# Kernel optimization log

Measured on AMD Instinct MI355X. Metric: run time of the kernel, lower is better.

## Reference

```python
import jax, jax.numpy as jnp
import numpy as np

B = 8192
EPS = 1e-5


def _bn(x, g, b):
    # BatchNorm1d in training mode: biased batch statistics
    m = jnp.mean(x, axis=0)
    v = jnp.mean((x - m) ** 2, axis=0)
    return g * (x - m) * jax.lax.rsqrt(v + EPS) + b


def setup_inputs() -> dict:
    key = jax.random.key(0)
    ks = jax.random.split(key, 24)
    w = lambda k, shape: jax.random.normal(k, shape, jnp.float32) * 0.02
    z = lambda shape: jnp.zeros(shape, jnp.float32)
    o = lambda shape: jnp.ones(shape, jnp.float32)
    inp = {"pred_vertices": jax.random.normal(ks[0], (B, 1723, 3), jnp.float32)}
    inp["W0"] = w(ks[1], (5169, 1024)); inp["b0"] = z(1024); inp["g0"] = o(1024); inp["be0"] = z(1024)
    inp["W1a"] = w(ks[2], (1024, 1024)); inp["b1a"] = z(1024); inp["g1a"] = o(1024); inp["be1a"] = z(1024)
    inp["W1b"] = w(ks[3], (1024, 1024)); inp["b1b"] = z(1024); inp["g1b"] = o(1024); inp["be1b"] = z(1024)
    inp["W2a"] = w(ks[4], (1024, 1024)); inp["b2a"] = z(1024); inp["g2a"] = o(1024); inp["be2a"] = z(1024)
    inp["W2b"] = w(ks[5], (1024, 1024)); inp["b2b"] = z(1024); inp["g2b"] = o(1024); inp["be2b"] = z(1024)
    inp["W3"] = w(ks[6], (1024, 226)); inp["b3"] = z(226)
    return inp


def reference(pred_vertices, W0, b0, g0, be0,
              W1a, b1a, g1a, be1a, W1b, b1b, g1b, be1b,
              W2a, b2a, g2a, be2a, W2b, b2b, g2b, be2b,
              W3, b3):
    bsz = pred_vertices.shape[0]
    x = pred_vertices.reshape(bsz, 1723 * 3)
    # FCBlock: Linear -> BN -> ReLU
    h = jax.nn.relu(_bn(x @ W0 + b0, g0, be0))
    # FCResBlock x2: relu(x + BN(Linear(relu(BN(Linear(x))))))
    t = jax.nn.relu(_bn(h @ W1a + b1a, g1a, be1a))
    t = _bn(t @ W1b + b1b, g1b, be1b)
    h = jax.nn.relu(h + t)
    t = jax.nn.relu(_bn(h @ W2a + b2a, g2a, be2a))
    t = _bn(t @ W2b + b2b, g2b, be2b)
    h = jax.nn.relu(h + t)
    out = h @ W3 + b3  # (B, 226)
    rot = out[:, :216].reshape(-1, 3, 3)  # (B*24, 3, 3)
    pred_betas = out[:, 216:]
    # Batched Procrustes orthogonalization: R = U V^T, then scale by det (no-grad)
    U, S, Vh = jnp.linalg.svd(rot, full_matrices=False)
    R = jnp.einsum('nij,njk->nik', U, Vh)
    det = jax.lax.stop_gradient(jnp.linalg.det(R))[:, None, None]
    pred_rotmat = (R * det).reshape(bsz, 24, 3, 3)
    return (pred_rotmat, pred_betas)
```

## Files before the change

kernel.cpp:

```cpp
#include <hip/hip_runtime.h>
#include <hip/hip_bf16.h>
#include <math.h>

typedef __attribute__((ext_vector_type(8))) _Float16 half8;
typedef __attribute__((ext_vector_type(4))) float floatx4;
typedef __attribute__((ext_vector_type(4))) unsigned short ushortx4;

__device__ __forceinline__ float hu2f(unsigned short u) {
    _Float16 h;
    __builtin_memcpy(&h, &u, 2);
    return (float)h;
}
__device__ __forceinline__ unsigned short f2hu(float x) {
    _Float16 h = (_Float16)x;
    unsigned short u;
    __builtin_memcpy(&u, &h, 2);
    return u;
}
__device__ __forceinline__ void split2(float a, unsigned short& s0,
                                       unsigned short& s1) {
    s0 = f2hu(a);
    float r1 = a - hu2f(s0);
    s1 = f2hu(r1);
}

typedef __attribute__((address_space(1))) unsigned int as1_u32;
typedef __attribute__((address_space(3))) unsigned int as3_u32;
__device__ __forceinline__ void gload16(const void* g, void* l) {
    __builtin_amdgcn_global_load_lds((const as1_u32*)g, (as3_u32*)l, 16, 0, 0);
}

__global__ __launch_bounds__(256) void wsplit2_kernel(
    const float* __restrict__ W, unsigned short* __restrict__ out,
    int Ktrue, int Kpad, int Ntrue, int Nalloc)
{
    __shared__ float T[32][33];
    const int tx = threadIdx.x & 31, ty = threadIdx.x >> 5;
    const int k0 = blockIdx.x * 32, n0 = blockIdx.y * 32;
#pragma unroll
    for (int i = 0; i < 4; i++) {
        int k = k0 + ty + 8 * i, n = n0 + tx;
        T[ty + 8 * i][tx] = (k < Ktrue && n < Ntrue) ? W[(size_t)k * Ntrue + n] : 0.f;
    }
    __syncthreads();
    const size_t PS = (size_t)Nalloc * Kpad;
#pragma unroll
    for (int i = 0; i < 4; i++) {
        int n = n0 + ty + 8 * i, k = k0 + tx;
        if (n < Nalloc) {
            unsigned short h0, h1;
            split2(T[tx][ty + 8 * i], h0, h1);
            size_t base = (size_t)n * Kpad + k;
            out[base] = h0;
            out[PS + base] = h1;
        }
    }
}

__global__ __launch_bounds__(256) void asplit2_kernel(
    const float* __restrict__ A, unsigned short* __restrict__ out,
    int Ka, int Kpad, int M)
{
    const int kq = Kpad >> 2;
    const int n = M * kq;
    int idx = blockIdx.x * 256 + threadIdx.x;
    if (idx >= n) return;
    int row = idx / kq, c4 = idx - row * kq;
    const size_t PS = (size_t)M * Kpad;
    ushortx4 o0, o1;
#pragma unroll
    for (int e = 0; e < 4; e++) {
        int col = c4 * 4 + e;
        float v = (col < Ka) ? A[(size_t)row * Ka + col] : 0.f;
        unsigned short a, b;
        split2(v, a, b);
        o0[e] = a; o1[e] = b;
    }
    size_t base = (size_t)row * Kpad + c4 * 4;
    *(ushortx4*)(out + base) = o0;
    *(ushortx4*)(out + PS + base) = o1;
}

__global__ __launch_bounds__(256, 3) void mfma_gemm_h(
    const unsigned short* __restrict__ Apl,
    const unsigned short* __restrict__ Bpl,
    const float* __restrict__ bias, float* __restrict__ C,
    float* __restrict__ part,
    int M, int N, int Kpad, int Nb)
{
    __shared__ __align__(16) unsigned short As[2][128][32];
    __shared__ __align__(16) unsigned short Bs[2][128][32];
    __shared__ float sstat[2][4][16][2];

    const int tid = threadIdx.x;
    const int lane = tid & 63;
    const int wave = tid >> 6;
    const int wm = (wave & 1) * 64, wn = (wave >> 1) * 64;

    const int gx = gridDim.x;
    const int nwg = gx * gridDim.y;
    const int id = blockIdx.y * gx + blockIdx.x;
    const int cpx = nwg >> 3;
    const int swz = (id & 7) * cpx + (id >> 3);
    const int bm = (swz / gx) * 128, bn = (swz % gx) * 128;

    const int l15 = lane & 15, q = lane >> 4;
    const size_t PSA = (size_t)M * Kpad;
    const size_t PSB = (size_t)Nb * Kpad;

    const int srow = lane >> 2;
    const int gslot = (lane & 3) ^ ((srow >> 1) & 3);
    const int rkey = (l15 >> 1) & 3;

    floatx4 acc[4][4] = {};

    for (int k0 = 0; k0 < Kpad; k0 += 32) {
#pragma unroll
        for (int i = 0; i < 8; i++) {
            int e = wave * 8 + i;
            int mat = e >> 4, p = (e >> 3) & 1, rb = (e & 7) << 4;
            if (mat == 0) {
                gload16(Apl + (size_t)p * PSA + (size_t)(bm + rb + srow) * Kpad
                            + (k0 + gslot * 8),
                        &As[p][rb][0]);
            } else {
                gload16(Bpl + (size_t)p * PSB + (size_t)(bn + rb + srow) * Kpad
                            + (k0 + gslot * 8),
                        &Bs[p][rb][0]);
            }
        }
        __syncthreads();

        half8 bfr[2][4];
#pragma unroll
        for (int p = 0; p < 2; p++)
#pragma unroll
            for (int ni = 0; ni < 4; ni++)
                bfr[p][ni] = *(const half8*)&Bs[p][wn + ni * 16 + l15][(q ^ rkey) * 8];
#pragma unroll
        for (int pa = 0; pa < 2; pa++) {
            half8 af[4];
#pragma unroll
            for (int mi = 0; mi < 4; mi++)
                af[mi] = *(const half8*)&As[pa][wm + mi * 16 + l15][(q ^ rkey) * 8];
#pragma unroll
            for (int pb = 0; pb + pa < 2; pb++) {
#pragma unroll
                for (int mi = 0; mi < 4; mi++)
#pragma unroll
                    for (int ni = 0; ni < 4; ni++)
                        acc[mi][ni] = __builtin_amdgcn_mfma_f32_16x16x32_f16(
                            af[mi], bfr[pb][ni], acc[mi][ni], 0, 0, 0);
            }
        }
        __syncthreads();
    }

    float ps[4], ps2[4];
#pragma unroll
    for (int ni = 0; ni < 4; ni++) {
        int col = bn + wn + ni * 16 + l15;
        float s = 0.f, s2 = 0.f;
        if (col < N) {
            float bv = bias[col];
#pragma unroll
            for (int mi = 0; mi < 4; mi++) {
#pragma unroll
                for (int reg = 0; reg < 4; reg++) {
                    int row = bm + wm + mi * 16 + q * 4 + reg;
                    float v = acc[mi][ni][reg] + bv;
                    C[(size_t)row * N + col] = v;
                    s += v;
                    s2 += v * v;
                }
            }
        }
        ps[ni] = s; ps2[ni] = s2;
    }

    if (part) {
#pragma unroll
        for (int ni = 0; ni < 4; ni++) {
            ps[ni]  += __shfl_xor(ps[ni], 16);  ps[ni]  += __shfl_xor(ps[ni], 32);
            ps2[ni] += __shfl_xor(ps2[ni], 16); ps2[ni] += __shfl_xor(ps2[ni], 32);
        }
        if (q == 0 && (wave & 1) == 1) {
#pragma unroll
            for (int ni = 0; ni < 4; ni++) {
                sstat[wave >> 1][ni][l15][0] = ps[ni];
                sstat[wave >> 1][ni][l15][1] = ps2[ni];
            }
        }
        __syncthreads();
        if (q == 0 && (wave & 1) == 0) {
            int chunk = bm >> 7;
#pragma unroll
            for (int ni = 0; ni < 4; ni++) {
                int col = bn + wn + ni * 16 + l15;
                float s  = ps[ni]  + sstat[wave >> 1][ni][l15][0];
                float s2 = ps2[ni] + sstat[wave >> 1][ni][l15][1];
                part[(size_t)(chunk * 2 + 0) * N + col] = s;
                part[(size_t)(chunk * 2 + 1) * N + col] = s2;
            }
        }
    }
}

template <bool AVEC, bool NV4>
__global__ __launch_bounds__(256) void gemm128(
    const float* __restrict__ A, const float* __restrict__ B,
    const float* __restrict__ bias, float* __restrict__ C,
    int M, int N, int Keff, int Ktrue, int Ka)
{
    __shared__ __align__(16) float Asm[16][132];
    __shared__ __align__(16) float Bsm[16][132];
    const int tid = threadIdx.x;
    const int bm = blockIdx.y * 128, bn = blockIdx.x * 128;
    const int tx = tid & 15, ty = tid >> 4;
    const int arow = tid >> 2, ac = tid & 3;
    const int bk = tid >> 4, bc = tid & 15;
    float acc[8][8] = {};
    for (int k0 = 0; k0 < Keff; k0 += 16) {
#pragma unroll
        for (int h = 0; h < 2; h++) {
            int rr = arow + h * 64;
            if (AVEC) {
                float4 v = *(const float4*)&A[(size_t)(bm + rr) * Ka + k0 + ac * 4];
                const float* pv = &v.x;
#pragma unroll
                for (int e = 0; e < 4; e++) Asm[ac * 4 + e][rr] = pv[e];
            } else {
#pragma unroll
                for (int e = 0; e < 4; e++) {
                    int kg = k0 + ac * 4 + e;
                    Asm[ac * 4 + e][rr] = (kg < Ka) ? A[(size_t)(bm + rr) * Ka + kg] : 0.f;
                }
            }
        }
        {
            int kg = k0 + bk;
            bool kok = (kg < Ktrue);
#pragma unroll
            for (int h = 0; h < 2; h++) {
                int cc = bc * 4 + h * 64;
                if (NV4) {
                    float4 v = {0.f, 0.f, 0.f, 0.f};
                    if (kok) v = *(const float4*)&B[(size_t)kg * N + bn + cc];
                    *(float4*)&Bsm[bk][cc] = v;
                } else {
#pragma unroll
                    for (int e = 0; e < 4; e++) {
                        int col = bn + cc + e;
                        Bsm[bk][cc + e] = (kok && col < N) ? B[(size_t)kg * N + col] : 0.f;
                    }
                }
            }
        }
        __syncthreads();
#pragma unroll
        for (int k = 0; k < 16; k++) {
            float4 a0 = *(const float4*)&Asm[k][ty * 4];
            float4 a1 = *(const float4*)&Asm[k][ty * 4 + 64];
            float4 b0 = *(const float4*)&Bsm[k][tx * 4];
            float4 b1 = *(const float4*)&Bsm[k][tx * 4 + 64];
            float av[8] = {a0.x, a0.y, a0.z, a0.w, a1.x, a1.y, a1.z, a1.w};
            float bv[8] = {b0.x, b0.y, b0.z, b0.w, b1.x, b1.y, b1.z, b1.w};
#pragma unroll
            for (int i = 0; i < 8; i++)
#pragma unroll
                for (int j = 0; j < 8; j++) acc[i][j] += av[i] * bv[j];
        }
        __syncthreads();
    }
#pragma unroll
    for (int i = 0; i < 8; i++) {
        int row = bm + (i < 4 ? ty * 4 + i : 64 + ty * 4 + (i - 4));
#pragma unroll
        for (int jh = 0; jh < 2; jh++)
#pragma unroll
            for (int e = 0; e < 4; e++) {
                int col = bn + jh * 64 + tx * 4 + e;
                if (NV4 || col < N)
                    C[(size_t)row * N + col] = acc[i][jh * 4 + e] + bias[col];
            }
    }
}

__global__ __launch_bounds__(256) void colstats_kernel(
    const float* __restrict__ Y, float* __restrict__ part, int N, int rows)
{
    int c = blockIdx.x * 256 + threadIdx.x;
    int r0 = blockIdx.y * rows;
    const float* p = Y + (size_t)r0 * N + c;
    float s = 0.f, s2 = 0.f;
    for (int r = 0; r < rows; r++) {
        float v = p[(size_t)r * N];
        s += v;
        s2 += v * v;
    }
    part[(size_t)(blockIdx.y * 2 + 0) * N + c] = s;
    part[(size_t)(blockIdx.y * 2 + 1) * N + c] = s2;
}

__global__ void finalize_stats_kernel(
    const float* __restrict__ part, const float* __restrict__ g,
    const float* __restrict__ be, float* __restrict__ scale,
    float* __restrict__ shift, int N, int nchunk, float invM)
{
    int c = blockIdx.x * blockDim.x + threadIdx.x;
    if (c >= N) return;
    float s = 0.f, s2 = 0.f;
    for (int i = 0; i < nchunk; i++) {
        s  += part[(size_t)(2 * i + 0) * N + c];
        s2 += part[(size_t)(2 * i + 1) * N + c];
    }
    float m = s * invM;
    float v = s2 * invM - m * m;
    if (v < 0.f) v = 0.f;
    float sc = g[c] / sqrtf(v + 1e-5f);
    scale[c] = sc;
    shift[c] = be[c] - m * sc;
}

__global__ __launch_bounds__(256) void bn_apply_kernel(
    float* __restrict__ Y, const float* __restrict__ scale,
    const float* __restrict__ shift, int do_relu, int write_y, int n4, int N,
    unsigned short* __restrict__ plane, size_t PS)
{
    int idx = blockIdx.x * 256 + threadIdx.x;
    if (idx >= n4) return;
    float4* Y4 = (float4*)Y;
    float4 v = Y4[idx];
    int c = (idx * 4) & (N - 1);
    v.x = v.x * scale[c + 0] + shift[c + 0];
    v.y = v.y * scale[c + 1] + shift[c + 1];
    v.z = v.z * scale[c + 2] + shift[c + 2];
    v.w = v.w * scale[c + 3] + shift[c + 3];
    if (do_relu) {
        v.x = fmaxf(v.x, 0.f); v.y = fmaxf(v.y, 0.f);
        v.z = fmaxf(v.z, 0.f); v.w = fmaxf(v.w, 0.f);
    }
    if (write_y) Y4[idx] = v;
    if (plane) {
        float vv[4] = {v.x, v.y, v.z, v.w};
        ushortx4 o0, o1;
#pragma unroll
        for (int e = 0; e < 4; e++) {
            unsigned short a, b;
            split2(vv[e], a, b);
            o0[e] = a; o1[e] = b;
        }
        size_t base = (size_t)idx * 4;
        *(ushortx4*)(plane + base) = o0;
        *(ushortx4*)(plane + PS + base) = o1;
    }
}

__global__ __launch_bounds__(256) void bn_resid_relu_kernel(
    float* __restrict__ Hb, const float* __restrict__ T,
    const float* __restrict__ scale, const float* __restrict__ shift,
    int n4, int N, unsigned short* __restrict__ plane, size_t PS)
{
    int idx = blockIdx.x * 256 + threadIdx.x;
    if (idx >= n4) return;
    float4 h = ((float4*)Hb)[idx];
    float4 t = ((const float4*)T)[idx];
    int c = (idx * 4) & (N - 1);
    t.x = t.x * scale[c + 0] + shift[c + 0];
    t.y = t.y * scale[c + 1] + shift[c + 1];
    t.z = t.z * scale[c + 2] + shift[c + 2];
    t.w = t.w * scale[c + 3] + shift[c + 3];
    h.x = fmaxf(h.x + t.x, 0.f);
    h.y = fmaxf(h.y + t.y, 0.f);
    h.z = fmaxf(h.z + t.z, 0.f);
    h.w = fmaxf(h.w + t.w, 0.f);
    ((float4*)Hb)[idx] = h;
    if (plane) {
        float vv[4] = {h.x, h.y, h.z, h.w};
        ushortx4 o0, o1;
#pragma unroll
        for (int e = 0; e < 4; e++) {
            unsigned short a, b;
            split2(vv[e], a, b);
            o0[e] = a; o1[e] = b;
        }
        size_t base = (size_t)idx * 4;
        *(ushortx4*)(plane + base) = o0;
        *(ushortx4*)(plane + PS + base) = o1;
    }
}

__global__ __launch_bounds__(256) void resid_relu_kernel(
    float* __restrict__ Hb, const float* __restrict__ T, int n4,
    unsigned short* __restrict__ plane, size_t PS)
{
    int idx = blockIdx.x * 256 + threadIdx.x;
    if (idx >= n4) return;
    float4 h = ((float4*)Hb)[idx];
    float4 t = ((const float4*)T)[idx];
    h.x = fmaxf(h.x + t.x, 0.f);
    h.y = fmaxf(h.y + t.y, 0.f);
    h.z = fmaxf(h.z + t.z, 0.f);
    h.w = fmaxf(h.w + t.w, 0.f);
    ((float4*)Hb)[idx] = h;
    if (plane) {
        float vv[4] = {h.x, h.y, h.z, h.w};
        ushortx4 o0, o1;
#pragma unroll
        for (int e = 0; e < 4; e++) {
            unsigned short a, b;
            split2(vv[e], a, b);
            o0[e] = a; o1[e] = b;
        }
        size_t base = (size_t)idx * 4;
        *(ushortx4*)(plane + base) = o0;
        *(ushortx4*)(plane + PS + base) = o1;
    }
}

__global__ __launch_bounds__(256) void svd_kernel(
    const float* __restrict__ O3, float* __restrict__ out, int nb)
{
    int gidx = blockIdx.x * 256 + threadIdx.x;
    if (gidx >= nb * 24) return;
    int row = gidx / 24;
    int j = gidx - row * 24;
    const float* rowp = O3 + (size_t)row * 226;
    const float* src = rowp + j * 9;

    double m[3][3];
#pragma unroll
    for (int r = 0; r < 3; r++)
#pragma unroll
        for (int c = 0; c < 3; c++) m[r][c] = (double)src[r * 3 + c];

    double a[3][3];
#pragma unroll
    for (int r = 0; r < 3; r++)
#pragma unroll
        for (int c = 0; c < 3; c++) {
            double s = 0.0;
#pragma unroll
            for (int k = 0; k < 3; k++) s += m[k][r] * m[k][c];
            a[r][c] = s;
        }

    double V[3][3] = {{1, 0, 0}, {0, 1, 0}, {0, 0, 1}};
    const int PP[3] = {0, 0, 1}, QQ[3] = {1, 2, 2};
    for (int sweep = 0; sweep < 8; sweep++) {
        for (int r3 = 0; r3 < 3; r3++) {
            int p = PP[r3], q = QQ[r3];
            double apq = a[p][q];
            if (fabs(apq) < 1e-60) continue;
            double tau = (a[q][q] - a[p][p]) / (2.0 * apq);
            double t = ((tau >= 0.0) ? 1.0 : -1.0) / (fabs(tau) + sqrt(1.0 + tau * tau));
            double c = 1.0 / sqrt(1.0 + t * t);
            double s = t * c;
#pragma unroll
            for (int k = 0; k < 3; k++) {
                double xp = a[p][k], xq = a[q][k];
                a[p][k] = c * xp - s * xq;
                a[q][k] = s * xp + c * xq;
            }
#pragma unroll
            for (int k = 0; k < 3; k++) {
                double xp = a[k][p], xq = a[k][q];
                a[k][p] = c * xp - s * xq;
                a[k][q] = s * xp + c * xq;
            }
#pragma unroll
            for (int k = 0; k < 3; k++) {
                double xp = V[k][p], xq = V[k][q];
                V[k][p] = c * xp - s * xq;
                V[k][q] = s * xp + c * xq;
            }
        }
    }

    double lam[3] = {a[0][0], a[1][1], a[2][2]};
    int i3 = 0;
    if (lam[1] < lam[i3]) i3 = 1;
    if (lam[2] < lam[i3]) i3 = 2;
    int i1 = (i3 + 1) % 3, i2 = (i3 + 2) % 3;

    double v1[3], v2[3], v3[3];
#pragma unroll
    for (int k = 0; k < 3; k++) {
        v1[k] = V[k][i1];
        v2[k] = V[k][i2];
        v3[k] = V[k][i3];
    }

    double u1[3], u2[3];
#pragma unroll
    for (int r = 0; r < 3; r++)
        u1[r] = m[r][0] * v1[0] + m[r][1] * v1[1] + m[r][2] * v1[2];
    double n1 = sqrt(u1[0] * u1[0] + u1[1] * u1[1] + u1[2] * u1[2]);
    double inv1 = (n1 > 1e-150) ? 1.0 / n1 : 0.0;
#pragma unroll
    for (int r = 0; r < 3; r++) u1[r] *= inv1;

#pragma unroll
    for (int r = 0; r < 3; r++)
        u2[r] = m[r][0] * v2[0] + m[r][1] * v2[1] + m[r][2] * v2[2];
    double d12 = u1[0] * u2[0] + u1[1] * u2[1] + u1[2] * u2[2];
#pragma unroll
    for (int r = 0; r < 3; r++) u2[r] -= d12 * u1[r];
    double n2 = sqrt(u2[0] * u2[0] + u2[1] * u2[1] + u2[2] * u2[2]);
    double inv2 = (n2 > 1e-150) ? 1.0 / n2 : 0.0;
#pragma unroll
    for (int r = 0; r < 3; r++) u2[r] *= inv2;

    double detM = m[0][0] * (m[1][1] * m[2][2] - m[1][2] * m[2][1])
                - m[0][1] * (m[1][0] * m[2][2] - m[1][2] * m[2][0])
                + m[0][2] * (m[1][0] * m[2][1] - m[1][1] * m[2][0]);
    double sgn = (detM >= 0.0) ? 1.0 : -1.0;
    double detV = v1[0] * (v2[1] * v3[2] - v2[2] * v3[1])
                - v1[1] * (v2[0] * v3[2] - v2[2] * v3[0])
                + v1[2] * (v2[0] * v3[1] - v2[1] * v3[0]);
    double sv = (detV >= 0.0) ? 1.0 : -1.0;

    double u3[3];
    u3[0] = sgn * sv * (u1[1] * u2[2] - u1[2] * u2[1]);
    u3[1] = sgn * sv * (u1[2] * u2[0] - u1[0] * u2[2]);
    u3[2] = sgn * sv * (u1[0] * u2[1] - u1[1] * u2[0]);

    size_t rot_base = (size_t)gidx * 9;
    size_t beta_base = (size_t)nb * 24 * 9 + (size_t)row * 10;
#pragma unroll
    for (int r = 0; r < 3; r++)
#pragma unroll
        for (int c = 0; c < 3; c++)
            out[rot_base + r * 3 + c] =
                (float)(sgn * (u1[r] * v1[c] + u2[r] * v2[c] + u3[r] * v3[c]));

    if (j < 10) out[beta_base + j] = rowp[216 + j];
}

extern "C" void kernel_launch(void* const* d_in, const int* in_sizes, int n_in,
                              void* d_out, int out_size, void* d_ws, size_t ws_size,
                              hipStream_t stream)
{
    const float* x    = (const float*)d_in[0];
    const float* W0   = (const float*)d_in[1];
    const float* b0   = (const float*)d_in[2];
    const float* g0   = (const float*)d_in[3];
    const float* be0  = (const float*)d_in[4];
    const float* W1a  = (const float*)d_in[5];
    const float* b1a  = (const float*)d_in[6];
    const float* g1a  = (const float*)d_in[7];
    const float* be1a = (const float*)d_in[8];
    const float* W1b  = (const float*)d_in[9];
    const float* b1b  = (const float*)d_in[10];
    const float* g1b  = (const float*)d_in[11];
    const float* be1b = (const float*)d_in[12];
    const float* W2a  = (const float*)d_in[13];
    const float* b2a  = (const float*)d_in[14];
    const float* g2a  = (const float*)d_in[15];
    const float* be2a = (const float*)d_in[16];
    const float* W2b  = (const float*)d_in[17];
    const float* b2b  = (const float*)d_in[18];
    const float* g2b  = (const float*)d_in[19];
    const float* be2b = (const float*)d_in[20];
    const float* W3   = (const float*)d_in[21];
    const float* b3   = (const float*)d_in[22];

    const int M = 8192, H = 1024, K0 = 5169, K0P = 5184, NO = 226, NOP = 256;
    const int NCH_NEW = 64;
    const int NCH_OLD = 32;

    const size_t SZ_ACT  = (size_t)M * H;
    const size_t SZ_O3   = (size_t)M * NO;
    const size_t SZ_PART = (size_t)2 * NCH_NEW * H;

    float* ws   = (float*)d_ws;
    float* buf0 = ws;
    float* buf1 = buf0 + SZ_ACT;
    float* buf2 = buf1 + SZ_ACT;
    float* buf3 = buf2 + SZ_ACT;
    float* part = buf3 + SZ_O3;
    float* scale = part + SZ_PART;
    float* shift = scale + H;
    size_t float_base = 3 * SZ_ACT + SZ_O3 + SZ_PART + 2 * H + 16;

    unsigned short* pl = (unsigned short*)(ws + float_base);
    unsigned short* w0p  = pl;
    unsigned short* w1ap = w0p  + (size_t)2 * H * K0P;
    unsigned short* w1bp = w1ap + (size_t)2 * H * H;
    unsigned short* w2ap = w1bp + (size_t)2 * H * H;
    unsigned short* w2bp = w2ap + (size_t)2 * H * H;
    unsigned short* w3p  = w2bp + (size_t)2 * H * H;
    unsigned short* xp  = w3p + (size_t)2 * NOP * H;
    unsigned short* a0p = xp  + (size_t)2 * M * K0P;
    unsigned short* a1p = a0p + (size_t)2 * M * H;
    unsigned short* pend = a1p + (size_t)2 * M * H;

    size_t bytes_new = float_base * 4 + (size_t)(pend - pl) * 2;
    bool use_new = ws_size >= bytes_new;

    dim3 blk(256);
    const int n4 = M * H / 4;
    const size_t PSH = (size_t)M * H;

    if (use_new) {
        wsplit2_kernel<<<dim3(K0P / 32, H / 32), blk, 0, stream>>>(W0, w0p, K0, K0P, H, H);
        wsplit2_kernel<<<dim3(H / 32, H / 32), blk, 0, stream>>>(W1a, w1ap, H, H, H, H);
        wsplit2_kernel<<<dim3(H / 32, H / 32), blk, 0, stream>>>(W1b, w1bp, H, H, H, H);
        wsplit2_kernel<<<dim3(H / 32, H / 32), blk, 0, stream>>>(W2a, w2ap, H, H, H, H);
        wsplit2_kernel<<<dim3(H / 32, H / 32), blk, 0, stream>>>(W2b, w2bp, H, H, H, H);
        wsplit2_kernel<<<dim3(H / 32, NOP / 32), blk, 0, stream>>>(W3, w3p, H, H, NO, NOP);
        asplit2_kernel<<<dim3(M * (K0P / 4) / 256), blk, 0, stream>>>(x, xp, K0, K0P, M);

        dim3 gH(H / 128, M / 128);
        dim3 gO(NOP / 128, M / 128);

        auto fin = [&](const float* g, const float* be) {
            finalize_stats_kernel<<<dim3(H / 256), blk, 0, stream>>>(
                part, g, be, scale, shift, H, NCH_NEW, 1.0f / M);
        };

        mfma_gemm_h<<<gH, blk, 0, stream>>>(xp, w0p, b0, buf0, part, M, H, K0P, H);
        fin(g0, be0);
        bn_apply_kernel<<<dim3(n4 / 256), blk, 0, stream>>>(buf0, scale, shift, 1, 1, n4, H, a0p, PSH);
        mfma_gemm_h<<<gH, blk, 0, stream>>>(a0p, w1ap, b1a, buf1, part, M, H, H, H);
        fin(g1a, be1a);
        bn_apply_kernel<<<dim3(n4 / 256), blk, 0, stream>>>(buf1, scale, shift, 1, 0, n4, H, a1p, PSH);
        mfma_gemm_h<<<gH, blk, 0, stream>>>(a1p, w1bp, b1b, buf2, part, M, H, H, H);
        fin(g1b, be1b);
        bn_resid_relu_kernel<<<dim3(n4 / 256), blk, 0, stream>>>(buf0, buf2, scale, shift, n4, H, a0p, PSH);
        mfma_gemm_h<<<gH, blk, 0, stream>>>(a0p, w2ap, b2a, buf1, part, M, H, H, H);
        fin(g2a, be2a);
        bn_apply_kernel<<<dim3(n4 / 256), blk, 0, stream>>>(buf1, scale, shift, 1, 0, n4, H, a1p, PSH);
        mfma_gemm_h<<<gH, blk, 0, stream>>>(a1p, w2bp, b2b, buf2, part, M, H, H, H);
        fin(g2b, be2b);
        bn_resid_relu_kernel<<<dim3(n4 / 256), blk, 0, stream>>>(buf0, buf2, scale, shift, n4, H, a0p, PSH);
        mfma_gemm_h<<<gO, blk, 0, stream>>>(a0p, w3p, b3, buf3, nullptr, M, NO, H, NOP);
    } else {
        auto bnstep = [&](float* Y, const float* g, const float* be, int relu) {
            colstats_kernel<<<dim3(H / 256, NCH_OLD), blk, 0, stream>>>(Y, part, H, M / NCH_OLD);
            finalize_stats_kernel<<<dim3(H / 256), blk, 0, stream>>>(part, g, be, scale, shift, H, NCH_OLD, 1.0f / M);
            bn_apply_kernel<<<dim3(n4 / 256), blk, 0, stream>>>(Y, scale, shift, relu, 1, n4, H, nullptr, 0);
        };
        dim3 gH(H / 128, M / 128);
        dim3 gO((NO + 127) / 128, M / 128);
        gemm128<false, true><<<gH, blk, 0, stream>>>(x, W0, b0, buf0, M, H, K0P, K0, K0);
        bnstep(buf0, g0, be0, 1);
        gemm128<true, true><<<gH, blk, 0, stream>>>(buf0, W1a, b1a, buf1, M, H, H, H, H);
        bnstep(buf1, g1a, be1a, 1);
        gemm128<true, true><<<gH, blk, 0, stream>>>(buf1, W1b, b1b, buf2, M, H, H, H, H);
        bnstep(buf2, g1b, be1b, 0);
        resid_relu_kernel<<<dim3(n4 / 256), blk, 0, stream>>>(buf0, buf2, n4, nullptr, 0);
        gemm128<true, true><<<gH, blk, 0, stream>>>(buf0, W2a, b2a, buf1, M, H, H, H, H);
        bnstep(buf1, g2a, be2a, 1);
        gemm128<true, true><<<gH, blk, 0, stream>>>(buf1, W2b, b2b, buf2, M, H, H, H, H);
        bnstep(buf2, g2b, be2b, 0);
        resid_relu_kernel<<<dim3(n4 / 256), blk, 0, stream>>>(buf0, buf2, n4, nullptr, 0);
        gemm128<true, false><<<gO, blk, 0, stream>>>(buf0, W3, b3, buf3, M, NO, H, H, H);
    }

    svd_kernel<<<dim3((M * 24 + 255) / 256), blk, 0, stream>>>(buf3, (float*)d_out, M);
}
```

Measured before the change: 1.116 ms.

## Accumulate BN stats via atomics, fuse finalize into apply, merge weight-split launches

The GEMM epilogue now adds its per-column sum and sum-of-squares straight into one global partial buffer per layer with atomicAdd, replacing per-chunk partials and the LDS reduction and barrier. The separate finalize_stats kernel is removed; each BN apply kernel recomputes scale and shift from the partials inline. The six weight-splitting launches are merged into a single kernel that dispatches on block index, and a memset zeroes the partial buffers. This cuts launch count and a small kernel per layer, at the cost of atomic contention and redundant per-thread coefficient math.

```diff
diff --git a/kernel.cpp b/kernel.cpp
--- a/kernel.cpp
+++ b/kernel.cpp
@@ -30,13 +30,11 @@
     __builtin_amdgcn_global_load_lds((const as1_u32*)g, (as3_u32*)l, 16, 0, 0);
 }
 
-__global__ __launch_bounds__(256) void wsplit2_kernel(
+__device__ __forceinline__ void wsplit_body(
     const float* __restrict__ W, unsigned short* __restrict__ out,
-    int Ktrue, int Kpad, int Ntrue, int Nalloc)
-{
-    __shared__ float T[32][33];
-    const int tx = threadIdx.x & 31, ty = threadIdx.x >> 5;
-    const int k0 = blockIdx.x * 32, n0 = blockIdx.y * 32;
+    int Ktrue, int Kpad, int Ntrue, int Nalloc, int k0, int n0,
+    float (*T)[33], int tx, int ty)
+{
 #pragma unroll
     for (int i = 0; i < 4; i++) {
         int k = k0 + ty + 8 * i, n = n0 + tx;
@@ -57,6 +55,43 @@
     }
 }
 
+__global__ __launch_bounds__(256) void wsplit_all_kernel(
+    const float* __restrict__ W0,  const float* __restrict__ W1a,
+    const float* __restrict__ W1b, const float* __restrict__ W2a,
+    const float* __restrict__ W2b, const float* __restrict__ W3,
+    unsigned short* __restrict__ w0p,  unsigned short* __restrict__ w1ap,
+    unsigned short* __restrict__ w1bp, unsigned short* __restrict__ w2ap,
+    unsigned short* __restrict__ w2bp, unsigned short* __restrict__ w3p)
+{
+    __shared__ float T[32][33];
+    const int tx = threadIdx.x & 31, ty = threadIdx.x >> 5;
+    int bid = blockIdx.x;
+    if (bid < 5184) {
+        wsplit_body(W0, w0p, 5169, 5184, 1024, 1024,
+                    (bid % 162) * 32, (bid / 162) * 32, T, tx, ty);
+    } else if (bid < 6208) {
+        int r = bid - 5184;
+        wsplit_body(W1a, w1ap, 1024, 1024, 1024, 1024,
+                    (r & 31) * 32, (r >> 5) * 32, T, tx, ty);
+    } else if (bid < 7232) {
+        int r = bid - 6208;
+        wsplit_body(W1b, w1bp, 1024, 1024, 1024, 1024,
+                    (r & 31) * 32, (r >> 5) * 32, T, tx, ty);
+    } else if (bid < 8256) {
+        int r = bid - 7232;
+        wsplit_body(W2a, w2ap, 1024, 1024, 1024, 1024,
+                    (r & 31) * 32, (r >> 5) * 32, T, tx, ty);
+    } else if (bid < 9280) {
+        int r = bid - 8256;
+        wsplit_body(W2b, w2bp, 1024, 1024, 1024, 1024,
+                    (r & 31) * 32, (r >> 5) * 32, T, tx, ty);
+    } else {
+        int r = bid - 9280;
+        wsplit_body(W3, w3p, 1024, 1024, 226, 256,
+                    (r & 31) * 32, (r >> 5) * 32, T, tx, ty);
+    }
+}
+
 __global__ __launch_bounds__(256) void asplit2_kernel(
     const float* __restrict__ A, unsigned short* __restrict__ out,
     int Ka, int Kpad, int M)
@@ -90,7 +125,6 @@
 {
     __shared__ __align__(16) unsigned short As[2][128][32];
     __shared__ __align__(16) unsigned short Bs[2][128][32];
-    __shared__ float sstat[2][4][16][2];
 
     const int tid = threadIdx.x;
     const int lane = tid & 63;
@@ -184,23 +218,14 @@
             ps[ni]  += __shfl_xor(ps[ni], 16);  ps[ni]  += __shfl_xor(ps[ni], 32);
             ps2[ni] += __shfl_xor(ps2[ni], 16); ps2[ni] += __shfl_xor(ps2[ni], 32);
         }
-        if (q == 0 && (wave & 1) == 1) {
-#pragma unroll
-            for (int ni = 0; ni < 4; ni++) {
-                sstat[wave >> 1][ni][l15][0] = ps[ni];
-                sstat[wave >> 1][ni][l15][1] = ps2[ni];
-            }
-        }
-        __syncthreads();
-        if (q == 0 && (wave & 1) == 0) {
-            int chunk = bm >> 7;
+        if (q == 0) {
 #pragma unroll
             for (int ni = 0; ni < 4; ni++) {
                 int col = bn + wn + ni * 16 + l15;
-                float s  = ps[ni]  + sstat[wave >> 1][ni][l15][0];
-                float s2 = ps2[ni] + sstat[wave >> 1][ni][l15][1];
-                part[(size_t)(chunk * 2 + 0) * N + col] = s;
-                part[(size_t)(chunk * 2 + 1) * N + col] = s2;
+                if (col < N) {
+                    atomicAdd(&part[col], ps[ni]);
+                    atomicAdd(&part[N + col], ps2[ni]);
+                }
             }
         }
     }
@@ -322,10 +347,9 @@
     shift[c] = be[c] - m * sc;
 }
 
-__global__ __launch_bounds__(256) void bn_apply_kernel(
+__global__ __launch_bounds__(256) void bn_apply_ss_kernel(
     float* __restrict__ Y, const float* __restrict__ scale,
-    const float* __restrict__ shift, int do_relu, int write_y, int n4, int N,
-    unsigned short* __restrict__ plane, size_t PS)
+    const float* __restrict__ shift, int do_relu, int n4, int N)
 {
     int idx = blockIdx.x * 256 + threadIdx.x;
     if (idx >= n4) return;
@@ -340,6 +364,51 @@
         v.x = fmaxf(v.x, 0.f); v.y = fmaxf(v.y, 0.f);
         v.z = fmaxf(v.z, 0.f); v.w = fmaxf(v.w, 0.f);
     }
+    Y4[idx] = v;
+}
+
+__device__ __forceinline__ void bn_coeff(
+    const float* __restrict__ part, const float* __restrict__ g,
+    const float* __restrict__ be, int c, float invM, float* sc, float* sh)
+{
+    float4 s4 = *(const float4*)&part[c];
+    float4 q4 = *(const float4*)&part[1024 + c];
+    float4 g4 = *(const float4*)&g[c];
+    float4 b4 = *(const float4*)&be[c];
+    const float* sp = &s4.x; const float* qp = &q4.x;
+    const float* gp = &g4.x; const float* bp = &b4.x;
+#pragma unroll
+    for (int e = 0; e < 4; e++) {
+        float m = sp[e] * invM;
+        float v = qp[e] * invM - m * m;
+        if (v < 0.f) v = 0.f;
+        float s = gp[e] / sqrtf(v + 1e-5f);
+        sc[e] = s;
+        sh[e] = bp[e] - m * s;
+    }
+}
+
+__global__ __launch_bounds__(256) void bn_apply_kernel(
+    float* __restrict__ Y, const float* __restrict__ part,
+    const float* __restrict__ g, const float* __restrict__ be,
+    int do_relu, int write_y, int n4, float invM,
+    unsigned short* __restrict__ plane, size_t PS)
+{
+    int idx = blockIdx.x * 256 + threadIdx.x;
+    if (idx >= n4) return;
+    float4* Y4 = (float4*)Y;
+    float4 v = Y4[idx];
+    int c = (idx * 4) & 1023;
+    float sc[4], sh[4];
+    bn_coeff(part, g, be, c, invM, sc, sh);
+    v.x = v.x * sc[0] + sh[0];
+    v.y = v.y * sc[1] + sh[1];
+    v.z = v.z * sc[2] + sh[2];
+    v.w = v.w * sc[3] + sh[3];
+    if (do_relu) {
+        v.x = fmaxf(v.x, 0.f); v.y = fmaxf(v.y, 0.f);
+        v.z = fmaxf(v.z, 0.f); v.w = fmaxf(v.w, 0.f);
+    }
     if (write_y) Y4[idx] = v;
     if (plane) {
         float vv[4] = {v.x, v.y, v.z, v.w};
@@ -358,18 +427,21 @@
 
 __global__ __launch_bounds__(256) void bn_resid_relu_kernel(
     float* __restrict__ Hb, const float* __restrict__ T,
-    const float* __restrict__ scale, const float* __restrict__ shift,
-    int n4, int N, unsigned short* __restrict__ plane, size_t PS)
+    const float* __restrict__ part, const float* __restrict__ g,
+    const float* __restrict__ be, int n4, float invM,
+    unsigned short* __restrict__ plane, size_t PS)
 {
     int idx = blockIdx.x * 256 + threadIdx.x;
     if (idx >= n4) return;
     float4 h = ((float4*)Hb)[idx];
     float4 t = ((const float4*)T)[idx];
-    int c = (idx * 4) & (N - 1);
-    t.x = t.x * scale[c + 0] + shift[c + 0];
-    t.y = t.y * scale[c + 1] + shift[c + 1];
-    t.z = t.z * scale[c + 2] + shift[c + 2];
-    t.w = t.w * scale[c + 3] + shift[c + 3];
+    int c = (idx * 4) & 1023;
+    float sc[4], sh[4];
+    bn_coeff(part, g, be, c, invM, sc, sh);
+    t.x = t.x * sc[0] + sh[0];
+    t.y = t.y * sc[1] + sh[1];
+    t.z = t.z * sc[2] + sh[2];
+    t.w = t.w * sc[3] + sh[3];
     h.x = fmaxf(h.x + t.x, 0.f);
     h.y = fmaxf(h.y + t.y, 0.f);
     h.z = fmaxf(h.z + t.z, 0.f);
@@ -391,8 +463,7 @@
 }
 
 __global__ __launch_bounds__(256) void resid_relu_kernel(
-    float* __restrict__ Hb, const float* __restrict__ T, int n4,
-    unsigned short* __restrict__ plane, size_t PS)
+    float* __restrict__ Hb, const float* __restrict__ T, int n4)
 {
     int idx = blockIdx.x * 256 + threadIdx.x;
     if (idx >= n4) return;
@@ -403,19 +474,6 @@
     h.z = fmaxf(h.z + t.z, 0.f);
     h.w = fmaxf(h.w + t.w, 0.f);
     ((float4*)Hb)[idx] = h;
-    if (plane) {
-        float vv[4] = {h.x, h.y, h.z, h.w};
-        ushortx4 o0, o1;
-#pragma unroll
-        for (int e = 0; e < 4; e++) {
-            unsigned short a, b;
-            split2(vv[e], a, b);
-            o0[e] = a; o1[e] = b;
-        }
-        size_t base = (size_t)idx * 4;
-        *(ushortx4*)(plane + base) = o0;
-        *(ushortx4*)(plane + PS + base) = o1;
-    }
 }
 
 __global__ __launch_bounds__(256) void svd_kernel(
@@ -566,20 +624,19 @@
     const float* b3   = (const float*)d_in[22];
 
     const int M = 8192, H = 1024, K0 = 5169, K0P = 5184, NO = 226, NOP = 256;
-    const int NCH_NEW = 64;
     const int NCH_OLD = 32;
 
     const size_t SZ_ACT  = (size_t)M * H;
     const size_t SZ_O3   = (size_t)M * NO;
-    const size_t SZ_PART = (size_t)2 * NCH_NEW * H;
+    const size_t SZ_PART = (size_t)2 * NCH_OLD * H;
 
     float* ws   = (float*)d_ws;
     float* buf0 = ws;
     float* buf1 = buf0 + SZ_ACT;
     float* buf2 = buf1 + SZ_ACT;
     float* buf3 = buf2 + SZ_ACT;
-    float* part = buf3 + SZ_O3;
-    float* scale = part + SZ_PART;
+    float* parts = buf3 + SZ_O3;
+    float* scale = parts + SZ_PART;
     float* shift = scale + H;
     size_t float_base = 3 * SZ_ACT + SZ_O3 + SZ_PART + 2 * H + 16;
 
@@ -601,45 +658,39 @@
     dim3 blk(256);
     const int n4 = M * H / 4;
     const size_t PSH = (size_t)M * H;
+    const float invM = 1.0f / M;
 
     if (use_new) {
-        wsplit2_kernel<<<dim3(K0P / 32, H / 32), blk, 0, stream>>>(W0, w0p, K0, K0P, H, H);
-        wsplit2_kernel<<<dim3(H / 32, H / 32), blk, 0, stream>>>(W1a, w1ap, H, H, H, H);
-        wsplit2_kernel<<<dim3(H / 32, H / 32), blk, 0, stream>>>(W1b, w1bp, H, H, H, H);
-        wsplit2_kernel<<<dim3(H / 32, H / 32), blk, 0, stream>>>(W2a, w2ap, H, H, H, H);
-        wsplit2_kernel<<<dim3(H / 32, H / 32), blk, 0, stream>>>(W2b, w2bp, H, H, H, H);
-        wsplit2_kernel<<<dim3(H / 32, NOP / 32), blk, 0, stream>>>(W3, w3p, H, H, NO, NOP);
+        float* p0 = parts + 0 * 2 * H;
+        float* p1 = parts + 1 * 2 * H;
+        float* p2 = parts + 2 * 2 * H;
+        float* p3 = parts + 3 * 2 * H;
+        float* p4 = parts + 4 * 2 * H;
+        hipMemsetAsync(parts, 0, (size_t)6 * 2 * H * sizeof(float), stream);
+
+        wsplit_all_kernel<<<dim3(9536), blk, 0, stream>>>(
+            W0, W1a, W1b, W2a, W2b, W3, w0p, w1ap, w1bp, w2ap, w2bp, w3p);
         asplit2_kernel<<<dim3(M * (K0P / 4) / 256), blk, 0, stream>>>(x, xp, K0, K0P, M);
 
         dim3 gH(H / 128, M / 128);
         dim3 gO(NOP / 128, M / 128);
 
-        auto fin = [&](const float* g, const float* be) {
-            finalize_stats_kernel<<<dim3(H / 256), blk, 0, stream>>>(
-                part, g, be, scale, shift, H, NCH_NEW, 1.0f / M);
-        };
-
-        mfma_gemm_h<<<gH, blk, 0, stream>>>(xp, w0p, b0, buf0, part, M, H, K0P, H);
-        fin(g0, be0);
-        bn_apply_kernel<<<dim3(n4 / 256), blk, 0, stream>>>(buf0, scale, shift, 1, 1, n4, H, a0p, PSH);
-        mfma_gemm_h<<<gH, blk, 0, stream>>>(a0p, w1ap, b1a, buf1, part, M, H, H, H);
-        fin(g1a, be1a);
-        bn_apply_kernel<<<dim3(n4 / 256), blk, 0, stream>>>(buf1, scale, shift, 1, 0, n4, H, a1p, PSH);
-        mfma_gemm_h<<<gH, blk, 0, stream>>>(a1p, w1bp, b1b, buf2, part, M, H, H, H);
-        fin(g1b, be1b);
-        bn_resid_relu_kernel<<<dim3(n4 / 256), blk, 0, stream>>>(buf0, buf2, scale, shift, n4, H, a0p, PSH);
-        mfma_gemm_h<<<gH, blk, 0, stream>>>(a0p, w2ap, b2a, buf1, part, M, H, H, H);
-        fin(g2a, be2a);
-        bn_apply_kernel<<<dim3(n4 / 256), blk, 0, stream>>>(buf1, scale, shift, 1, 0, n4, H, a1p, PSH);
-        mfma_gemm_h<<<gH, blk, 0, stream>>>(a1p, w2bp, b2b, buf2, part, M, H, H, H);
-        fin(g2b, be2b);
-        bn_resid_relu_kernel<<<dim3(n4 / 256), blk, 0, stream>>>(buf0, buf2, scale, shift, n4, H, a0p, PSH);
+        mfma_gemm_h<<<gH, blk, 0, stream>>>(xp, w0p, b0, buf0, p0, M, H, K0P, H);
+        bn_apply_kernel<<<dim3(n4 / 256), blk, 0, stream>>>(buf0, p0, g0, be0, 1, 1, n4, invM, a0p, PSH);
+        mfma_gemm_h<<<gH, blk, 0, stream>>>(a0p, w1ap, b1a, buf1, p1, M, H, H, H);
+        bn_apply_kernel<<<dim3(n4 / 256), blk, 0, stream>>>(buf1, p1, g1a, be1a, 1, 0, n4, invM, a1p, PSH);
+        mfma_gemm_h<<<gH, blk, 0, stream>>>(a1p, w1bp, b1b, buf2, p2, M, H, H, H);
+        bn_resid_relu_kernel<<<dim3(n4 / 256), blk, 0, stream>>>(buf0, buf2, p2, g1b, be1b, n4, invM, a0p, PSH);
+        mfma_gemm_h<<<gH, blk, 0, stream>>>(a0p, w2ap, b2a, buf1, p3, M, H, H, H);
+        bn_apply_kernel<<<dim3(n4 / 256), blk, 0, stream>>>(buf1, p3, g2a, be2a, 1, 0, n4, invM, a1p, PSH);
+        mfma_gemm_h<<<gH, blk, 0, stream>>>(a1p, w2bp, b2b, buf2, p4, M, H, H, H);
+        bn_resid_relu_kernel<<<dim3(n4 / 256), blk, 0, stream>>>(buf0, buf2, p4, g2b, be2b, n4, invM, a0p, PSH);
         mfma_gemm_h<<<gO, blk, 0, stream>>>(a0p, w3p, b3, buf3, nullptr, M, NO, H, NOP);
     } else {
         auto bnstep = [&](float* Y, const float* g, const float* be, int relu) {
-            colstats_kernel<<<dim3(H / 256, NCH_OLD), blk, 0, stream>>>(Y, part, H, M / NCH_OLD);
-            finalize_stats_kernel<<<dim3(H / 256), blk, 0, stream>>>(part, g, be, scale, shift, H, NCH_OLD, 1.0f / M);
-            bn_apply_kernel<<<dim3(n4 / 256), blk, 0, stream>>>(Y, scale, shift, relu, 1, n4, H, nullptr, 0);
+            colstats_kernel<<<dim3(H / 256, NCH_OLD), blk, 0, stream>>>(Y, parts, H, M / NCH_OLD);
+            finalize_stats_kernel<<<dim3(H / 256), blk, 0, stream>>>(parts, g, be, scale, shift, H, NCH_OLD, invM);
+            bn_apply_ss_kernel<<<dim3(n4 / 256), blk, 0, stream>>>(Y, scale, shift, relu, n4, H);
         };
         dim3 gH(H / 128, M / 128);
         dim3 gO((NO + 127) / 128, M / 128);
@@ -649,12 +700,12 @@
         bnstep(buf1, g1a, be1a, 1);
         gemm128<true, true><<<gH, blk, 0, stream>>>(buf1, W1b, b1b, buf2, M, H, H, H, H);
         bnstep(buf2, g1b, be1b, 0);
-        resid_relu_kernel<<<dim3(n4 / 256), blk, 0, stream>>>(buf0, buf2, n4, nullptr, 0);
+        resid_relu_kernel<<<dim3(n4 / 256), blk, 0, stream>>>(buf0, buf2, n4);
         gemm128<true, true><<<gH, blk, 0, stream>>>(buf0, W2a, b2a, buf1, M, H, H, H, H);
         bnstep(buf1, g2a, be2a, 1);
         gemm128<true, true><<<gH, blk, 0, stream>>>(buf1, W2b, b2b, buf2, M, H, H, H, H);
         bnstep(buf2, g2b, be2b, 0);
-        resid_relu_kernel<<<dim3(n4 / 256), blk, 0, stream>>>(buf0, buf2, n4, nullptr, 0);
+        resid_relu_kernel<<<dim3(n4 / 256), blk, 0, stream>>>(buf0, buf2, n4);
         gemm128<true, false><<<gO, blk, 0, stream>>>(buf0, W3, b3, buf3, M, NO, H, H, H);
     }
 
```

Result: faster. 1.023 ms (-8.3%).
